# Performance work log

Hardware: AMD Instinct MI355X
Metric: run time of the kernel (lower is better)

The kernel has to match this reference:

```python
import jax, jax.numpy as jnp
import numpy as np

N_NODES = 100000
N_EDGES = 1600000
D_IN = 64
D_HID = 64
EPS = 0.0  # dgl GINConv default: init_eps=0, learn_eps=False


def setup_inputs() -> dict:
    key = jax.random.key(0)
    k1, k2, k3, k4, k5 = jax.random.split(key, 5)
    x = jax.random.normal(k1, (N_NODES, D_IN), dtype=jnp.float32)
    src = jax.random.randint(k2, (N_EDGES,), 0, N_NODES, dtype=jnp.int32)
    dst = jax.random.randint(k3, (N_EDGES,), 0, N_NODES, dtype=jnp.int32)
    # nn.Linear-style init scale
    W1 = jax.random.normal(k4, (D_IN, D_HID), dtype=jnp.float32) / np.sqrt(D_IN)
    b1 = jnp.zeros((D_HID,), dtype=jnp.float32)
    W2 = jax.random.normal(k5, (D_HID, D_HID), dtype=jnp.float32) / np.sqrt(D_HID)
    b2 = jnp.zeros((D_HID,), dtype=jnp.float32)
    return {"x": x, "src": src, "dst": dst, "W1": W1, "b1": b1, "W2": W2, "b2": b2}


def _gin_layer(h, src, dst, W, b):
    # sum-aggregate messages from src -> dst (graph SpMM), then (1+eps)*h + agg,
    # then dense linear + ReLU — matches dgl GINConv(aggregator_type='sum', activation=ReLU)
    agg = jax.ops.segment_sum(h[src], dst, num_segments=N_NODES)  # [N, D]
    return jax.nn.relu(((1.0 + EPS) * h + agg) @ W + b)


def reference(x, src, dst, W1, b1, W2, b2):
    h = _gin_layer(x, src, dst, W1, b1)
    h = _gin_layer(h, src, dst, W2, b2)
    return h
```

## Files before the change

kernel.cpp:

```cpp
#include <hip/hip_runtime.h>
#include <hip/hip_bf16.h>


#define D 64
#define ROWS_PER_BLOCK 32
#define CHSZ 8192
#define NPBS 512
#define SBSHIFT 9
#define MAXNBS 256
#define MAXNCH 512

typedef unsigned short ushort_t;

__device__ inline unsigned short f2bf(float f) {
    unsigned u = __float_as_uint(f);
    return (unsigned short)((u + 0x7fff + ((u >> 16) & 1)) >> 16);
}

__device__ inline void acc8(float* acc, uint4 v) {
    acc[0] += __uint_as_float(v.x << 16);
    acc[1] += __uint_as_float(v.x & 0xffff0000u);
    acc[2] += __uint_as_float(v.y << 16);
    acc[3] += __uint_as_float(v.y & 0xffff0000u);
    acc[4] += __uint_as_float(v.z << 16);
    acc[5] += __uint_as_float(v.z & 0xffff0000u);
    acc[6] += __uint_as_float(v.w << 16);
    acc[7] += __uint_as_float(v.w & 0xffff0000u);
}


__global__ __launch_bounds__(256) void k1_hist(const int* __restrict__ dst,
                                               int* __restrict__ hist,
                                               int n_edges, int nch, int nbs) {
    __shared__ int lh[MAXNBS];
    for (int i = threadIdx.x; i < nbs; i += 256) lh[i] = 0;
    __syncthreads();
    int base = blockIdx.x * CHSZ;
    int lim = min(CHSZ, n_edges - base);
    for (int k = threadIdx.x; k < lim; k += 256)
        atomicAdd(&lh[dst[base + k] >> SBSHIFT], 1);
    __syncthreads();
    for (int i = threadIdx.x; i < nbs; i += 256)
        hist[i * nch + blockIdx.x] = lh[i];
}

__global__ __launch_bounds__(256) void k2a_rowsum(const int* __restrict__ hist,
                                                  int* __restrict__ total,
                                                  int nch, int nbs) {
    int w = threadIdx.x >> 6;
    int lane = threadIdx.x & 63;
    int b = blockIdx.x * 4 + w;
    if (b >= nbs) return;
    const int* row = hist + (size_t)b * nch;
    int s = 0;
    for (int c = lane; c < nch; c += 64) s += row[c];
#pragma unroll
    for (int off = 32; off > 0; off >>= 1) s += __shfl_down(s, off);
    if (lane == 0) total[b] = s;
}

__global__ __launch_bounds__(256) void k2b_scan(const int* __restrict__ total,
                                                int* __restrict__ sstart,
                                                int nbs, int n_edges) {
    __shared__ int t[256];
    int tid = threadIdx.x;
    t[tid] = (tid < nbs) ? total[tid] : 0;
    __syncthreads();
    for (int off = 1; off < 256; off <<= 1) {
        int v = (tid >= off) ? t[tid - off] : 0;
        __syncthreads();
        t[tid] += v;
        __syncthreads();
    }
    if (tid < nbs) sstart[tid] = (tid == 0) ? 0 : t[tid - 1];
    if (tid == 0) sstart[nbs] = n_edges;
}

__global__ __launch_bounds__(256) void k2c_rowscan(int* __restrict__ hist,
                                                   const int* __restrict__ sstart,
                                                   int nch, int nbs) {
    __shared__ int t[MAXNCH];
    int b = blockIdx.x;
    int tid = threadIdx.x;
    int* row = hist + (size_t)b * nch;
    int nround = (nch + 255) & ~255;
    for (int i = tid; i < nround; i += 256) t[i] = (i < nch) ? row[i] : 0;
    __syncthreads();
    for (int off = 1; off < nround; off <<= 1) {
        int v[MAXNCH / 256];
        for (int i = tid, j = 0; i < nround; i += 256, ++j)
            v[j] = (i >= off) ? t[i - off] : 0;
        __syncthreads();
        for (int i = tid, j = 0; i < nround; i += 256, ++j) t[i] += v[j];
        __syncthreads();
    }
    int base = sstart[b];
    for (int i = tid; i < nch; i += 256)
        row[i] = base + ((i == 0) ? 0 : t[i - 1]);
}

__global__ __launch_bounds__(256) void k3_scatter(const int* __restrict__ src,
                                                  const int* __restrict__ dst,
                                                  const int* __restrict__ hist,
                                                  unsigned* __restrict__ tmp,
                                                  int n_edges, int nch, int nbs) {
    __shared__ int lcur[MAXNBS];
    int c = blockIdx.x;
    for (int i = threadIdx.x; i < nbs; i += 256) lcur[i] = hist[i * nch + c];
    __syncthreads();
    int base = c * CHSZ;
    int lim = min(CHSZ, n_edges - base);
    for (int k = threadIdx.x; k < lim; k += 256) {
        int d = dst[base + k];
        int s = src[base + k];
        int pos = atomicAdd(&lcur[d >> SBSHIFT], 1);
        tmp[pos] = ((unsigned)(d & (NPBS - 1)) << 18) | (unsigned)s;
    }
}

__global__ __launch_bounds__(256) void k4_fine(const unsigned* __restrict__ tmp,
                                               const int* __restrict__ sstart,
                                               int* __restrict__ esrc,
                                               int* __restrict__ offs,
                                               int n_nodes) {
    __shared__ int lcnt[NPBS];
    __shared__ int lcur[NPBS];
    __shared__ int tsum[256];

    int b = blockIdx.x;
    int tid = threadIdx.x;
    int base = sstart[b];
    int cnt = sstart[b + 1] - base;

    lcnt[tid] = 0; lcnt[tid + 256] = 0;
    __syncthreads();

    for (int i = tid; i < cnt; i += 256)
        atomicAdd(&lcnt[tmp[base + i] >> 18], 1);
    __syncthreads();

    int a0 = lcnt[2 * tid], a1 = lcnt[2 * tid + 1];
    tsum[tid] = a0 + a1;
    __syncthreads();
    for (int off = 1; off < 256; off <<= 1) {
        int v = (tid >= off) ? tsum[tid - off] : 0;
        __syncthreads();
        tsum[tid] += v;
        __syncthreads();
    }
    int ex = (tid == 0) ? 0 : tsum[tid - 1];
    lcur[2 * tid] = ex;
    lcur[2 * tid + 1] = ex + a0;

    int node = b * NPBS + 2 * tid;
    if (node <= n_nodes) offs[node] = base + ex;
    if (node + 1 <= n_nodes) offs[node + 1] = base + ex + a0;
    __syncthreads();

    for (int i = tid; i < cnt; i += 256) {
        unsigned p = tmp[base + i];
        int pos = atomicAdd(&lcur[p >> 18], 1);
        esrc[base + pos] = (int)(p & 0x3FFFFu);
    }
}


__global__ __launch_bounds__(256) void to_bf16(const float4* __restrict__ in,
                                               uint2* __restrict__ out, int n4) {
    int i = blockIdx.x * 256 + threadIdx.x;
    if (i >= n4) return;
    float4 v = in[i];
    out[i] = make_uint2((unsigned)f2bf(v.x) | ((unsigned)f2bf(v.y) << 16),
                        (unsigned)f2bf(v.z) | ((unsigned)f2bf(v.w) << 16));
}

__global__ __launch_bounds__(256) void gin_agg_bf(const uint4* __restrict__ hb,
                                                  const int* __restrict__ offs,
                                                  const int* __restrict__ esrc,
                                                  float4* __restrict__ agg,
                                                  int n_nodes) {
    int t = blockIdx.x * 256 + threadIdx.x;
    int n = t >> 2;
    if (n >= n_nodes) return;
    int c = t & 3;
    const uint4* self = hb + (size_t)n * 8 + c * 2;
    float acc[16];
#pragma unroll
    for (int j = 0; j < 16; ++j) acc[j] = 0.0f;
    uint4 sv0 = self[0], sv1 = self[1];
    acc8(acc, sv0); acc8(acc + 8, sv1);

    int i = offs[n];
    int end = offs[n + 1];
    for (; i + 4 <= end; i += 4) {
        const uint4* r0 = hb + (size_t)esrc[i]     * 8 + c * 2;
        const uint4* r1 = hb + (size_t)esrc[i + 1] * 8 + c * 2;
        const uint4* r2 = hb + (size_t)esrc[i + 2] * 8 + c * 2;
        const uint4* r3 = hb + (size_t)esrc[i + 3] * 8 + c * 2;
        uint4 a0 = r0[0], b0 = r0[1];
        uint4 a1 = r1[0], b1 = r1[1];
        uint4 a2 = r2[0], b2 = r2[1];
        uint4 a3 = r3[0], b3 = r3[1];
        acc8(acc, a0); acc8(acc + 8, b0);
        acc8(acc, a1); acc8(acc + 8, b1);
        acc8(acc, a2); acc8(acc + 8, b2);
        acc8(acc, a3); acc8(acc + 8, b3);
    }
    for (; i < end; ++i) {
        const uint4* r = hb + (size_t)esrc[i] * 8 + c * 2;
        uint4 a = r[0], b = r[1];
        acc8(acc, a); acc8(acc + 8, b);
    }

    float4* o = agg + (size_t)n * 16 + c * 4;
    o[0] = make_float4(acc[0], acc[1], acc[2], acc[3]);
    o[1] = make_float4(acc[4], acc[5], acc[6], acc[7]);
    o[2] = make_float4(acc[8], acc[9], acc[10], acc[11]);
    o[3] = make_float4(acc[12], acc[13], acc[14], acc[15]);
}

template <bool BF16OUT>
__global__ __launch_bounds__(256) void gin_mlp(const float* __restrict__ hs,
                                               const float* __restrict__ W,
                                               const float* __restrict__ b,
                                               void* __restrict__ out_,
                                               int n_nodes) {
    __shared__ float Wl[D * D];
    __shared__ float bl[D];
    __shared__ float rows[ROWS_PER_BLOCK][D];

    int tid = threadIdx.x;

    const float4* W4 = (const float4*)W;
    float4* Wl4 = (float4*)Wl;
#pragma unroll
    for (int i = 0; i < 4; ++i) Wl4[tid + 256 * i] = W4[tid + 256 * i];
    if (tid < D / 4) ((float4*)bl)[tid] = ((const float4*)b)[tid];

    size_t row0 = (size_t)blockIdx.x * ROWS_PER_BLOCK;
    const float4* hs4 = (const float4*)(hs + row0 * D);
    float4* rows4 = (float4*)rows;
#pragma unroll
    for (int i = 0; i < 2; ++i) rows4[tid + 256 * i] = hs4[tid + 256 * i];

    __syncthreads();

    int lane = tid & 63;
    int w = tid >> 6;

    float acc[8];
#pragma unroll
    for (int r = 0; r < 8; ++r) acc[r] = bl[lane];

#pragma unroll
    for (int k = 0; k < D; ++k) {
        float wv = Wl[k * D + lane];
#pragma unroll
        for (int r = 0; r < 8; ++r)
            acc[r] = fmaf(rows[w * 8 + r][k], wv, acc[r]);
    }

#pragma unroll
    for (int r = 0; r < 8; ++r) {
        float v = acc[r] > 0.0f ? acc[r] : 0.0f;
        size_t idx = (row0 + (size_t)w * 8 + r) * D + lane;
        if (BF16OUT) ((ushort_t*)out_)[idx] = f2bf(v);
        else         ((float*)out_)[idx] = v;
    }
}

extern "C" void kernel_launch(void* const* d_in, const int* in_sizes, int n_in,
                              void* d_out, int out_size, void* d_ws, size_t ws_size,
                              hipStream_t stream) {
    const float* x   = (const float*)d_in[0];
    const int*   src = (const int*)d_in[1];
    const int*   dst = (const int*)d_in[2];
    const float* W1  = (const float*)d_in[3];
    const float* b1  = (const float*)d_in[4];
    const float* W2  = (const float*)d_in[5];
    const float* b2  = (const float*)d_in[6];
    float* out = (float*)d_out;

    const int n_nodes = in_sizes[0] / D;
    const int n_edges = in_sizes[1];
    const int nch = (n_edges + CHSZ - 1) / CHSZ;
    const int nbs = (n_nodes + NPBS - 1) / NPBS;

    float*    A      = (float*)d_ws;
    ushort_t* hb     = (ushort_t*)(A + (size_t)n_nodes * D);
    int*      offs   = (int*)(hb + (size_t)n_nodes * D);
    int*      sstart = offs + (n_nodes + 1);
    int*      total  = sstart + (nbs + 1);
    int*      hist   = total + nbs;
    unsigned* tmp    = (unsigned*)(hist + (size_t)nbs * nch);
    int*      esrc   = (int*)(tmp + n_edges);

    const int agg_blocks = (n_nodes * 4 + 255) / 256;
    const int mlp_blocks = (n_nodes + ROWS_PER_BLOCK - 1) / ROWS_PER_BLOCK;
    const int cvt_blocks = (n_nodes * (D / 4) + 255) / 256;

    k1_hist<<<nch, 256, 0, stream>>>(dst, hist, n_edges, nch, nbs);
    k2a_rowsum<<<(nbs + 3) / 4, 256, 0, stream>>>(hist, total, nch, nbs);
    k2b_scan<<<1, 256, 0, stream>>>(total, sstart, nbs, n_edges);
    k2c_rowscan<<<nbs, 256, 0, stream>>>(hist, sstart, nch, nbs);
    k3_scatter<<<nch, 256, 0, stream>>>(src, dst, hist, tmp, n_edges, nch, nbs);
    k4_fine<<<nbs, 256, 0, stream>>>(tmp, sstart, esrc, offs, n_nodes);

    to_bf16<<<cvt_blocks, 256, 0, stream>>>((const float4*)x, (uint2*)hb,
                                            n_nodes * (D / 4));
    gin_agg_bf<<<agg_blocks, 256, 0, stream>>>((const uint4*)hb, offs, esrc,
                                               (float4*)A, n_nodes);
    gin_mlp<true><<<mlp_blocks, 256, 0, stream>>>(A, W1, b1, hb, n_nodes);

    gin_agg_bf<<<agg_blocks, 256, 0, stream>>>((const uint4*)hb, offs, esrc,
                                               (float4*)A, n_nodes);
    gin_mlp<false><<<mlp_blocks, 256, 0, stream>>>(A, W2, b2, out, n_nodes);
}
```

Before: 196.4 us.

## Fuse aggregation into MLP and group nodes by degree for balanced work

```diff
diff --git a/kernel.cpp b/kernel.cpp
--- a/kernel.cpp
+++ b/kernel.cpp
@@ -3,12 +3,13 @@
 
 
 #define D 64
-#define ROWS_PER_BLOCK 32
+#define RPB 32
 #define CHSZ 8192
 #define NPBS 512
 #define SBSHIFT 9
 #define MAXNBS 256
 #define MAXNCH 512
+#define DBINS 256
 
 typedef unsigned short ushort_t;
 
@@ -29,8 +30,15 @@
 }
 
 
+__global__ void zero_small(int* __restrict__ total, int* __restrict__ degcnt, int nbs) {
+    int i = threadIdx.x;
+    for (int j = i; j < nbs; j += 256) total[j] = 0;
+    for (int j = i; j < DBINS; j += 256) degcnt[j] = 0;
+}
+
 __global__ __launch_bounds__(256) void k1_hist(const int* __restrict__ dst,
                                                int* __restrict__ hist,
+                                               int* __restrict__ total,
                                                int n_edges, int nch, int nbs) {
     __shared__ int lh[MAXNBS];
     for (int i = threadIdx.x; i < nbs; i += 256) lh[i] = 0;
@@ -40,23 +48,11 @@
     for (int k = threadIdx.x; k < lim; k += 256)
         atomicAdd(&lh[dst[base + k] >> SBSHIFT], 1);
     __syncthreads();
-    for (int i = threadIdx.x; i < nbs; i += 256)
-        hist[i * nch + blockIdx.x] = lh[i];
-}
-
-__global__ __launch_bounds__(256) void k2a_rowsum(const int* __restrict__ hist,
-                                                  int* __restrict__ total,
-                                                  int nch, int nbs) {
-    int w = threadIdx.x >> 6;
-    int lane = threadIdx.x & 63;
-    int b = blockIdx.x * 4 + w;
-    if (b >= nbs) return;
-    const int* row = hist + (size_t)b * nch;
-    int s = 0;
-    for (int c = lane; c < nch; c += 64) s += row[c];
-#pragma unroll
-    for (int off = 32; off > 0; off >>= 1) s += __shfl_down(s, off);
-    if (lane == 0) total[b] = s;
+    for (int i = threadIdx.x; i < nbs; i += 256) {
+        int v = lh[i];
+        hist[i * nch + blockIdx.x] = v;
+        if (v) atomicAdd(&total[i], v);
+    }
 }
 
 __global__ __launch_bounds__(256) void k2b_scan(const int* __restrict__ total,
@@ -122,10 +118,12 @@
                                                const int* __restrict__ sstart,
                                                int* __restrict__ esrc,
                                                int* __restrict__ offs,
+                                               int* __restrict__ degcnt,
                                                int n_nodes) {
     __shared__ int lcnt[NPBS];
     __shared__ int lcur[NPBS];
     __shared__ int tsum[256];
+    __shared__ int dcnt[DBINS];
 
     int b = blockIdx.x;
     int tid = threadIdx.x;
@@ -133,6 +131,7 @@
     int cnt = sstart[b + 1] - base;
 
     lcnt[tid] = 0; lcnt[tid + 256] = 0;
+    dcnt[tid] = 0;
     __syncthreads();
 
     for (int i = tid; i < cnt; i += 256)
@@ -140,6 +139,9 @@
     __syncthreads();
 
     int a0 = lcnt[2 * tid], a1 = lcnt[2 * tid + 1];
+    int node = b * NPBS + 2 * tid;
+    if (node < n_nodes)     atomicAdd(&dcnt[min(a0, DBINS - 1)], 1);
+    if (node + 1 < n_nodes) atomicAdd(&dcnt[min(a1, DBINS - 1)], 1);
     tsum[tid] = a0 + a1;
     __syncthreads();
     for (int off = 1; off < 256; off <<= 1) {
@@ -152,16 +154,53 @@
     lcur[2 * tid] = ex;
     lcur[2 * tid + 1] = ex + a0;
 
-    int node = b * NPBS + 2 * tid;
     if (node <= n_nodes) offs[node] = base + ex;
     if (node + 1 <= n_nodes) offs[node + 1] = base + ex + a0;
     __syncthreads();
+
+    if (dcnt[tid]) atomicAdd(&degcnt[tid], dcnt[tid]);
 
     for (int i = tid; i < cnt; i += 256) {
         unsigned p = tmp[base + i];
         int pos = atomicAdd(&lcur[p >> 18], 1);
         esrc[base + pos] = (int)(p & 0x3FFFFu);
     }
+}
+
+__global__ __launch_bounds__(256) void degscan(const int* __restrict__ degcnt,
+                                               int* __restrict__ degcur) {
+    __shared__ int t[DBINS];
+    int tid = threadIdx.x;
+    t[tid] = degcnt[tid];
+    __syncthreads();
+    for (int off = 1; off < 256; off <<= 1) {
+        int v = (tid >= off) ? t[tid - off] : 0;
+        __syncthreads();
+        t[tid] += v;
+        __syncthreads();
+    }
+    degcur[tid] = (tid == 0) ? 0 : t[tid - 1];
+}
+
+__global__ __launch_bounds__(256) void degscatter(const int* __restrict__ offs,
+                                                  int* __restrict__ degcur,
+                                                  int* __restrict__ perm,
+                                                  int n_nodes) {
+    __shared__ int lcnt[DBINS];
+    __shared__ int lbase[DBINS];
+    int tid = threadIdx.x;
+    int n = blockIdx.x * 256 + tid;
+    lcnt[tid] = 0;
+    __syncthreads();
+    int bin = -1, lpos = 0;
+    if (n < n_nodes) {
+        bin = min(offs[n + 1] - offs[n], DBINS - 1);
+        lpos = atomicAdd(&lcnt[bin], 1);
+    }
+    __syncthreads();
+    if (lcnt[tid]) lbase[tid] = atomicAdd(&degcur[tid], lcnt[tid]);
+    __syncthreads();
+    if (n < n_nodes) perm[lbase[bin] + lpos] = n;
 }
 
 
@@ -174,60 +213,19 @@
                         (unsigned)f2bf(v.z) | ((unsigned)f2bf(v.w) << 16));
 }
 
-__global__ __launch_bounds__(256) void gin_agg_bf(const uint4* __restrict__ hb,
-                                                  const int* __restrict__ offs,
-                                                  const int* __restrict__ esrc,
-                                                  float4* __restrict__ agg,
-                                                  int n_nodes) {
-    int t = blockIdx.x * 256 + threadIdx.x;
-    int n = t >> 2;
-    if (n >= n_nodes) return;
-    int c = t & 3;
-    const uint4* self = hb + (size_t)n * 8 + c * 2;
-    float acc[16];
-#pragma unroll
-    for (int j = 0; j < 16; ++j) acc[j] = 0.0f;
-    uint4 sv0 = self[0], sv1 = self[1];
-    acc8(acc, sv0); acc8(acc + 8, sv1);
-
-    int i = offs[n];
-    int end = offs[n + 1];
-    for (; i + 4 <= end; i += 4) {
-        const uint4* r0 = hb + (size_t)esrc[i]     * 8 + c * 2;
-        const uint4* r1 = hb + (size_t)esrc[i + 1] * 8 + c * 2;
-        const uint4* r2 = hb + (size_t)esrc[i + 2] * 8 + c * 2;
-        const uint4* r3 = hb + (size_t)esrc[i + 3] * 8 + c * 2;
-        uint4 a0 = r0[0], b0 = r0[1];
-        uint4 a1 = r1[0], b1 = r1[1];
-        uint4 a2 = r2[0], b2 = r2[1];
-        uint4 a3 = r3[0], b3 = r3[1];
-        acc8(acc, a0); acc8(acc + 8, b0);
-        acc8(acc, a1); acc8(acc + 8, b1);
-        acc8(acc, a2); acc8(acc + 8, b2);
-        acc8(acc, a3); acc8(acc + 8, b3);
-    }
-    for (; i < end; ++i) {
-        const uint4* r = hb + (size_t)esrc[i] * 8 + c * 2;
-        uint4 a = r[0], b = r[1];
-        acc8(acc, a); acc8(acc + 8, b);
-    }
-
-    float4* o = agg + (size_t)n * 16 + c * 4;
-    o[0] = make_float4(acc[0], acc[1], acc[2], acc[3]);
-    o[1] = make_float4(acc[4], acc[5], acc[6], acc[7]);
-    o[2] = make_float4(acc[8], acc[9], acc[10], acc[11]);
-    o[3] = make_float4(acc[12], acc[13], acc[14], acc[15]);
-}
-
 template <bool BF16OUT>
-__global__ __launch_bounds__(256) void gin_mlp(const float* __restrict__ hs,
-                                               const float* __restrict__ W,
-                                               const float* __restrict__ b,
-                                               void* __restrict__ out_,
-                                               int n_nodes) {
+__global__ __launch_bounds__(256) void gin_layer(const uint4* __restrict__ hb,
+                                                 const int* __restrict__ offs,
+                                                 const int* __restrict__ esrc,
+                                                 const int* __restrict__ perm,
+                                                 const float* __restrict__ W,
+                                                 const float* __restrict__ bias,
+                                                 void* __restrict__ out_,
+                                                 int n_nodes) {
     __shared__ float Wl[D * D];
     __shared__ float bl[D];
-    __shared__ float rows[ROWS_PER_BLOCK][D];
+    __shared__ float rows[RPB][D];
+    __shared__ int pn[RPB];
 
     int tid = threadIdx.x;
 
@@ -235,35 +233,58 @@
     float4* Wl4 = (float4*)Wl;
 #pragma unroll
     for (int i = 0; i < 4; ++i) Wl4[tid + 256 * i] = W4[tid + 256 * i];
-    if (tid < D / 4) ((float4*)bl)[tid] = ((const float4*)b)[tid];
-
-    size_t row0 = (size_t)blockIdx.x * ROWS_PER_BLOCK;
-    const float4* hs4 = (const float4*)(hs + row0 * D);
-    float4* rows4 = (float4*)rows;
-#pragma unroll
-    for (int i = 0; i < 2; ++i) rows4[tid + 256 * i] = hs4[tid + 256 * i];
-
+    if (tid < D / 4) ((float4*)bl)[tid] = ((const float4*)bias)[tid];
+    if (tid < RPB) {
+        int r = blockIdx.x * RPB + tid;
+        pn[tid] = (r < n_nodes) ? perm[r] : -1;
+    }
+    __syncthreads();
+
+    int g = tid >> 3;
+    int l = tid & 7;
+    int n = pn[g];
+    float acc[8];
+#pragma unroll
+    for (int j = 0; j < 8; ++j) acc[j] = 0.0f;
+    if (n >= 0) {
+        acc8(acc, hb[(size_t)n * 8 + l]);
+        int i = offs[n];
+        int end = offs[n + 1];
+        for (; i + 4 <= end; i += 4) {
+            uint4 v0 = hb[(size_t)esrc[i]     * 8 + l];
+            uint4 v1 = hb[(size_t)esrc[i + 1] * 8 + l];
+            uint4 v2 = hb[(size_t)esrc[i + 2] * 8 + l];
+            uint4 v3 = hb[(size_t)esrc[i + 3] * 8 + l];
+            acc8(acc, v0); acc8(acc, v1); acc8(acc, v2); acc8(acc, v3);
+        }
+        for (; i < end; ++i)
+            acc8(acc, hb[(size_t)esrc[i] * 8 + l]);
+    }
+#pragma unroll
+    for (int j = 0; j < 8; ++j) rows[g][l * 8 + j] = acc[j];
     __syncthreads();
 
     int lane = tid & 63;
     int w = tid >> 6;
 
-    float acc[8];
-#pragma unroll
-    for (int r = 0; r < 8; ++r) acc[r] = bl[lane];
+    float macc[8];
+#pragma unroll
+    for (int r = 0; r < 8; ++r) macc[r] = bl[lane];
 
 #pragma unroll
     for (int k = 0; k < D; ++k) {
         float wv = Wl[k * D + lane];
 #pragma unroll
         for (int r = 0; r < 8; ++r)
-            acc[r] = fmaf(rows[w * 8 + r][k], wv, acc[r]);
+            macc[r] = fmaf(rows[w * 8 + r][k], wv, macc[r]);
     }
 
 #pragma unroll
     for (int r = 0; r < 8; ++r) {
-        float v = acc[r] > 0.0f ? acc[r] : 0.0f;
-        size_t idx = (row0 + (size_t)w * 8 + r) * D + lane;
+        int nr = pn[w * 8 + r];
+        if (nr < 0) continue;
+        float v = macc[r] > 0.0f ? macc[r] : 0.0f;
+        size_t idx = (size_t)nr * D + lane;
         if (BF16OUT) ((ushort_t*)out_)[idx] = f2bf(v);
         else         ((float*)out_)[idx] = v;
     }
@@ -286,33 +307,36 @@
     const int nch = (n_edges + CHSZ - 1) / CHSZ;
     const int nbs = (n_nodes + NPBS - 1) / NPBS;
 
-    float*    A      = (float*)d_ws;
-    ushort_t* hb     = (ushort_t*)(A + (size_t)n_nodes * D);
-    int*      offs   = (int*)(hb + (size_t)n_nodes * D);
+    ushort_t* xb     = (ushort_t*)d_ws;
+    ushort_t* h1b    = xb + (size_t)n_nodes * D;
+    int*      offs   = (int*)(h1b + (size_t)n_nodes * D);
     int*      sstart = offs + (n_nodes + 1);
     int*      total  = sstart + (nbs + 1);
-    int*      hist   = total + nbs;
-    unsigned* tmp    = (unsigned*)(hist + (size_t)nbs * nch);
+    int*      degcnt = total + nbs;
+    int*      degcur = degcnt + DBINS;
+    int*      hist   = degcur + DBINS;
+    int*      perm   = hist + (size_t)nbs * nch;
+    unsigned* tmp    = (unsigned*)(perm + n_nodes);
     int*      esrc   = (int*)(tmp + n_edges);
 
-    const int agg_blocks = (n_nodes * 4 + 255) / 256;
-    const int mlp_blocks = (n_nodes + ROWS_PER_BLOCK - 1) / ROWS_PER_BLOCK;
+    const int layer_blocks = (n_nodes + RPB - 1) / RPB;
     const int cvt_blocks = (n_nodes * (D / 4) + 255) / 256;
-
-    k1_hist<<<nch, 256, 0, stream>>>(dst, hist, n_edges, nch, nbs);
-    k2a_rowsum<<<(nbs + 3) / 4, 256, 0, stream>>>(hist, total, nch, nbs);
+    const int nscat_blocks = (n_nodes + 255) / 256;
+
+    zero_small<<<1, 256, 0, stream>>>(total, degcnt, nbs);
+    k1_hist<<<nch, 256, 0, stream>>>(dst, hist, total, n_edges, nch, nbs);
     k2b_scan<<<1, 256, 0, stream>>>(total, sstart, nbs, n_edges);
     k2c_rowscan<<<nbs, 256, 0, stream>>>(hist, sstart, nch, nbs);
     k3_scatter<<<nch, 256, 0, stream>>>(src, dst, hist, tmp, n_edges, nch, nbs);
-    k4_fine<<<nbs, 256, 0, stream>>>(tmp, sstart, esrc, offs, n_nodes);
-
-    to_bf16<<<cvt_blocks, 256, 0, stream>>>((const float4*)x, (uint2*)hb,
+    k4_fine<<<nbs, 256, 0, stream>>>(tmp, sstart, esrc, offs, degcnt, n_nodes);
+    degscan<<<1, 256, 0, stream>>>(degcnt, degcur);
+    degscatter<<<nscat_blocks, 256, 0, stream>>>(offs, degcur, perm, n_nodes);
+
+    to_bf16<<<cvt_blocks, 256, 0, stream>>>((const float4*)x, (uint2*)xb,
                                             n_nodes * (D / 4));
-    gin_agg_bf<<<agg_blocks, 256, 0, stream>>>((const uint4*)hb, offs, esrc,
-                                               (float4*)A, n_nodes);
-    gin_mlp<true><<<mlp_blocks, 256, 0, stream>>>(A, W1, b1, hb, n_nodes);
-
-    gin_agg_bf<<<agg_blocks, 256, 0, stream>>>((const uint4*)hb, offs, esrc,
-                                               (float4*)A, n_nodes);
-    gin_mlp<false><<<mlp_blocks, 256, 0, stream>>>(A, W2, b2, out, n_nodes);
-}
+    gin_layer<true><<<layer_blocks, 256, 0, stream>>>((const uint4*)xb, offs, esrc,
+                                                      perm, W1, b1, h1b, n_nodes);
+
+    gin_layer<false><<<layer_blocks, 256, 0, stream>>>((const uint4*)h1b, offs, esrc,
+                                                       perm, W2, b2, out, n_nodes);
+}
```

Result: slower. 462.0 us (+135.2%).

## Sort nodes by in-degree for load-balanced aggregation; fold row-sum into histogram

Applied to the files above, without the earlier changes.

```diff
diff --git a/kernel.cpp b/kernel.cpp
--- a/kernel.cpp
+++ b/kernel.cpp
@@ -9,6 +9,7 @@
 #define SBSHIFT 9
 #define MAXNBS 256
 #define MAXNCH 512
+#define DBINS 256
 
 typedef unsigned short ushort_t;
 
@@ -29,8 +30,15 @@
 }
 
 
+__global__ void zero_small(int* __restrict__ total, int* __restrict__ degcnt, int nbs) {
+    int i = threadIdx.x;
+    for (int j = i; j < nbs; j += 256) total[j] = 0;
+    for (int j = i; j < DBINS; j += 256) degcnt[j] = 0;
+}
+
 __global__ __launch_bounds__(256) void k1_hist(const int* __restrict__ dst,
                                                int* __restrict__ hist,
+                                               int* __restrict__ total,
                                                int n_edges, int nch, int nbs) {
     __shared__ int lh[MAXNBS];
     for (int i = threadIdx.x; i < nbs; i += 256) lh[i] = 0;
@@ -40,23 +48,11 @@
     for (int k = threadIdx.x; k < lim; k += 256)
         atomicAdd(&lh[dst[base + k] >> SBSHIFT], 1);
     __syncthreads();
-    for (int i = threadIdx.x; i < nbs; i += 256)
-        hist[i * nch + blockIdx.x] = lh[i];
-}
-
-__global__ __launch_bounds__(256) void k2a_rowsum(const int* __restrict__ hist,
-                                                  int* __restrict__ total,
-                                                  int nch, int nbs) {
-    int w = threadIdx.x >> 6;
-    int lane = threadIdx.x & 63;
-    int b = blockIdx.x * 4 + w;
-    if (b >= nbs) return;
-    const int* row = hist + (size_t)b * nch;
-    int s = 0;
-    for (int c = lane; c < nch; c += 64) s += row[c];
-#pragma unroll
-    for (int off = 32; off > 0; off >>= 1) s += __shfl_down(s, off);
-    if (lane == 0) total[b] = s;
+    for (int i = threadIdx.x; i < nbs; i += 256) {
+        int v = lh[i];
+        hist[i * nch + blockIdx.x] = v;
+        if (v) atomicAdd(&total[i], v);
+    }
 }
 
 __global__ __launch_bounds__(256) void k2b_scan(const int* __restrict__ total,
@@ -122,10 +118,12 @@
                                                const int* __restrict__ sstart,
                                                int* __restrict__ esrc,
                                                int* __restrict__ offs,
+                                               int* __restrict__ degcnt,
                                                int n_nodes) {
     __shared__ int lcnt[NPBS];
     __shared__ int lcur[NPBS];
     __shared__ int tsum[256];
+    __shared__ int dcnt[DBINS];
 
     int b = blockIdx.x;
     int tid = threadIdx.x;
@@ -133,6 +131,7 @@
     int cnt = sstart[b + 1] - base;
 
     lcnt[tid] = 0; lcnt[tid + 256] = 0;
+    dcnt[tid] = 0;
     __syncthreads();
 
     for (int i = tid; i < cnt; i += 256)
@@ -140,6 +139,9 @@
     __syncthreads();
 
     int a0 = lcnt[2 * tid], a1 = lcnt[2 * tid + 1];
+    int node = b * NPBS + 2 * tid;
+    if (node < n_nodes)     atomicAdd(&dcnt[min(a0, DBINS - 1)], 1);
+    if (node + 1 < n_nodes) atomicAdd(&dcnt[min(a1, DBINS - 1)], 1);
     tsum[tid] = a0 + a1;
     __syncthreads();
     for (int off = 1; off < 256; off <<= 1) {
@@ -152,16 +154,53 @@
     lcur[2 * tid] = ex;
     lcur[2 * tid + 1] = ex + a0;
 
-    int node = b * NPBS + 2 * tid;
     if (node <= n_nodes) offs[node] = base + ex;
     if (node + 1 <= n_nodes) offs[node + 1] = base + ex + a0;
     __syncthreads();
+
+    if (dcnt[tid]) atomicAdd(&degcnt[tid], dcnt[tid]);
 
     for (int i = tid; i < cnt; i += 256) {
         unsigned p = tmp[base + i];
         int pos = atomicAdd(&lcur[p >> 18], 1);
         esrc[base + pos] = (int)(p & 0x3FFFFu);
     }
+}
+
+__global__ __launch_bounds__(256) void degscan(const int* __restrict__ degcnt,
+                                               int* __restrict__ degcur) {
+    __shared__ int t[DBINS];
+    int tid = threadIdx.x;
+    t[tid] = degcnt[tid];
+    __syncthreads();
+    for (int off = 1; off < 256; off <<= 1) {
+        int v = (tid >= off) ? t[tid - off] : 0;
+        __syncthreads();
+        t[tid] += v;
+        __syncthreads();
+    }
+    degcur[tid] = (tid == 0) ? 0 : t[tid - 1];
+}
+
+__global__ __launch_bounds__(256) void degscatter(const int* __restrict__ offs,
+                                                  int* __restrict__ degcur,
+                                                  int* __restrict__ perm,
+                                                  int n_nodes) {
+    __shared__ int lcnt[DBINS];
+    __shared__ int lbase[DBINS];
+    int tid = threadIdx.x;
+    int n = blockIdx.x * 256 + tid;
+    lcnt[tid] = 0;
+    __syncthreads();
+    int bin = -1, lpos = 0;
+    if (n < n_nodes) {
+        bin = min(offs[n + 1] - offs[n], DBINS - 1);
+        lpos = atomicAdd(&lcnt[bin], 1);
+    }
+    __syncthreads();
+    if (lcnt[tid]) lbase[tid] = atomicAdd(&degcur[tid], lcnt[tid]);
+    __syncthreads();
+    if (n < n_nodes) perm[lbase[bin] + lpos] = n;
 }
 
 
@@ -177,11 +216,13 @@
 __global__ __launch_bounds__(256) void gin_agg_bf(const uint4* __restrict__ hb,
                                                   const int* __restrict__ offs,
                                                   const int* __restrict__ esrc,
+                                                  const int* __restrict__ perm,
                                                   float4* __restrict__ agg,
                                                   int n_nodes) {
     int t = blockIdx.x * 256 + threadIdx.x;
-    int n = t >> 2;
-    if (n >= n_nodes) return;
+    int nidx = t >> 2;
+    if (nidx >= n_nodes) return;
+    int n = perm[nidx];
     int c = t & 3;
     const uint4* self = hb + (size_t)n * 8 + c * 2;
     float acc[16];
@@ -291,28 +332,34 @@
     int*      offs   = (int*)(hb + (size_t)n_nodes * D);
     int*      sstart = offs + (n_nodes + 1);
     int*      total  = sstart + (nbs + 1);
-    int*      hist   = total + nbs;
-    unsigned* tmp    = (unsigned*)(hist + (size_t)nbs * nch);
+    int*      degcnt = total + nbs;
+    int*      degcur = degcnt + DBINS;
+    int*      hist   = degcur + DBINS;
+    int*      perm   = hist + (size_t)nbs * nch;
+    unsigned* tmp    = (unsigned*)(perm + n_nodes);
     int*      esrc   = (int*)(tmp + n_edges);
 
     const int agg_blocks = (n_nodes * 4 + 255) / 256;
     const int mlp_blocks = (n_nodes + ROWS_PER_BLOCK - 1) / ROWS_PER_BLOCK;
     const int cvt_blocks = (n_nodes * (D / 4) + 255) / 256;
-
-    k1_hist<<<nch, 256, 0, stream>>>(dst, hist, n_edges, nch, nbs);
-    k2a_rowsum<<<(nbs + 3) / 4, 256, 0, stream>>>(hist, total, nch, nbs);
+    const int nscat_blocks = (n_nodes + 255) / 256;
+
+    zero_small<<<1, 256, 0, stream>>>(total, degcnt, nbs);
+    k1_hist<<<nch, 256, 0, stream>>>(dst, hist, total, n_edges, nch, nbs);
     k2b_scan<<<1, 256, 0, stream>>>(total, sstart, nbs, n_edges);
     k2c_rowscan<<<nbs, 256, 0, stream>>>(hist, sstart, nch, nbs);
     k3_scatter<<<nch, 256, 0, stream>>>(src, dst, hist, tmp, n_edges, nch, nbs);
-    k4_fine<<<nbs, 256, 0, stream>>>(tmp, sstart, esrc, offs, n_nodes);
+    k4_fine<<<nbs, 256, 0, stream>>>(tmp, sstart, esrc, offs, degcnt, n_nodes);
+    degscan<<<1, 256, 0, stream>>>(degcnt, degcur);
+    degscatter<<<nscat_blocks, 256, 0, stream>>>(offs, degcur, perm, n_nodes);
 
     to_bf16<<<cvt_blocks, 256, 0, stream>>>((const float4*)x, (uint2*)hb,
                                             n_nodes * (D / 4));
     gin_agg_bf<<<agg_blocks, 256, 0, stream>>>((const uint4*)hb, offs, esrc,
-                                               (float4*)A, n_nodes);
+                                               perm, (float4*)A, n_nodes);
     gin_mlp<true><<<mlp_blocks, 256, 0, stream>>>(A, W1, b1, hb, n_nodes);
 
     gin_agg_bf<<<agg_blocks, 256, 0, stream>>>((const uint4*)hb, offs, esrc,
-                                               (float4*)A, n_nodes);
+                                               perm, (float4*)A, n_nodes);
     gin_mlp<false><<<mlp_blocks, 256, 0, stream>>>(A, W2, b2, out, n_nodes);
 }
```

Result: slower. 217.5 us (+10.7%).

## Store aggregates as bf16 and fold the histogram prefix into fewer launches

Applied to the files above, without the earlier changes.

```diff
diff --git a/kernel.cpp b/kernel.cpp
--- a/kernel.cpp
+++ b/kernel.cpp
@@ -28,9 +28,29 @@
     acc[7] += __uint_as_float(v.w & 0xffff0000u);
 }
 
+__device__ inline void unpack8(float* v, uint4 u) {
+    v[0] = __uint_as_float(u.x << 16); v[1] = __uint_as_float(u.x & 0xffff0000u);
+    v[2] = __uint_as_float(u.y << 16); v[3] = __uint_as_float(u.y & 0xffff0000u);
+    v[4] = __uint_as_float(u.z << 16); v[5] = __uint_as_float(u.z & 0xffff0000u);
+    v[6] = __uint_as_float(u.w << 16); v[7] = __uint_as_float(u.w & 0xffff0000u);
+}
+
+
+__global__ __launch_bounds__(256) void to_bf16z(const float4* __restrict__ in,
+                                                uint2* __restrict__ out, int n4,
+                                                int* __restrict__ total, int nbs) {
+    int i = blockIdx.x * 256 + threadIdx.x;
+    if (blockIdx.x == 0)
+        for (int j = threadIdx.x; j < nbs; j += 256) total[j] = 0;
+    if (i >= n4) return;
+    float4 v = in[i];
+    out[i] = make_uint2((unsigned)f2bf(v.x) | ((unsigned)f2bf(v.y) << 16),
+                        (unsigned)f2bf(v.z) | ((unsigned)f2bf(v.w) << 16));
+}
 
 __global__ __launch_bounds__(256) void k1_hist(const int* __restrict__ dst,
                                                int* __restrict__ hist,
+                                               int* __restrict__ total,
                                                int n_edges, int nch, int nbs) {
     __shared__ int lh[MAXNBS];
     for (int i = threadIdx.x; i < nbs; i += 256) lh[i] = 0;
@@ -40,48 +60,36 @@
     for (int k = threadIdx.x; k < lim; k += 256)
         atomicAdd(&lh[dst[base + k] >> SBSHIFT], 1);
     __syncthreads();
-    for (int i = threadIdx.x; i < nbs; i += 256)
-        hist[i * nch + blockIdx.x] = lh[i];
-}
-
-__global__ __launch_bounds__(256) void k2a_rowsum(const int* __restrict__ hist,
-                                                  int* __restrict__ total,
-                                                  int nch, int nbs) {
-    int w = threadIdx.x >> 6;
-    int lane = threadIdx.x & 63;
-    int b = blockIdx.x * 4 + w;
-    if (b >= nbs) return;
-    const int* row = hist + (size_t)b * nch;
-    int s = 0;
-    for (int c = lane; c < nch; c += 64) s += row[c];
-#pragma unroll
-    for (int off = 32; off > 0; off >>= 1) s += __shfl_down(s, off);
-    if (lane == 0) total[b] = s;
-}
-
-__global__ __launch_bounds__(256) void k2b_scan(const int* __restrict__ total,
-                                                int* __restrict__ sstart,
-                                                int nbs, int n_edges) {
-    __shared__ int t[256];
-    int tid = threadIdx.x;
-    t[tid] = (tid < nbs) ? total[tid] : 0;
-    __syncthreads();
-    for (int off = 1; off < 256; off <<= 1) {
-        int v = (tid >= off) ? t[tid - off] : 0;
-        __syncthreads();
-        t[tid] += v;
-        __syncthreads();
-    }
-    if (tid < nbs) sstart[tid] = (tid == 0) ? 0 : t[tid - 1];
-    if (tid == 0) sstart[nbs] = n_edges;
+    for (int i = threadIdx.x; i < nbs; i += 256) {
+        int v = lh[i];
+        hist[i * nch + blockIdx.x] = v;
+        if (v) atomicAdd(&total[i], v);
+    }
 }
 
 __global__ __launch_bounds__(256) void k2c_rowscan(int* __restrict__ hist,
-                                                   const int* __restrict__ sstart,
-                                                   int nch, int nbs) {
+                                                   const int* __restrict__ total,
+                                                   int* __restrict__ sstart,
+                                                   int nch, int nbs, int n_edges) {
+    __shared__ int tt[256];
     __shared__ int t[MAXNCH];
     int b = blockIdx.x;
     int tid = threadIdx.x;
+
+    tt[tid] = (tid < nbs) ? total[tid] : 0;
+    __syncthreads();
+    for (int off = 1; off < 256; off <<= 1) {
+        int v = (tid >= off) ? tt[tid - off] : 0;
+        __syncthreads();
+        tt[tid] += v;
+        __syncthreads();
+    }
+    int base = (b == 0) ? 0 : tt[b - 1];
+    if (tid == 0) {
+        sstart[b] = base;
+        if (b == 0) sstart[nbs] = n_edges;
+    }
+
     int* row = hist + (size_t)b * nch;
     int nround = (nch + 255) & ~255;
     for (int i = tid; i < nround; i += 256) t[i] = (i < nch) ? row[i] : 0;
@@ -94,7 +102,6 @@
         for (int i = tid, j = 0; i < nround; i += 256, ++j) t[i] += v[j];
         __syncthreads();
     }
-    int base = sstart[b];
     for (int i = tid; i < nch; i += 256)
         row[i] = base + ((i == 0) ? 0 : t[i - 1]);
 }
@@ -165,19 +172,10 @@
 }
 
 
-__global__ __launch_bounds__(256) void to_bf16(const float4* __restrict__ in,
-                                               uint2* __restrict__ out, int n4) {
-    int i = blockIdx.x * 256 + threadIdx.x;
-    if (i >= n4) return;
-    float4 v = in[i];
-    out[i] = make_uint2((unsigned)f2bf(v.x) | ((unsigned)f2bf(v.y) << 16),
-                        (unsigned)f2bf(v.z) | ((unsigned)f2bf(v.w) << 16));
-}
-
 __global__ __launch_bounds__(256) void gin_agg_bf(const uint4* __restrict__ hb,
                                                   const int* __restrict__ offs,
                                                   const int* __restrict__ esrc,
-                                                  float4* __restrict__ agg,
+                                                  uint4* __restrict__ aggb,
                                                   int n_nodes) {
     int t = blockIdx.x * 256 + threadIdx.x;
     int n = t >> 2;
@@ -212,22 +210,29 @@
         acc8(acc, a); acc8(acc + 8, b);
     }
 
-    float4* o = agg + (size_t)n * 16 + c * 4;
-    o[0] = make_float4(acc[0], acc[1], acc[2], acc[3]);
-    o[1] = make_float4(acc[4], acc[5], acc[6], acc[7]);
-    o[2] = make_float4(acc[8], acc[9], acc[10], acc[11]);
-    o[3] = make_float4(acc[12], acc[13], acc[14], acc[15]);
-}
-
+    uint4 o0, o1;
+    o0.x = (unsigned)f2bf(acc[0])  | ((unsigned)f2bf(acc[1])  << 16);
+    o0.y = (unsigned)f2bf(acc[2])  | ((unsigned)f2bf(acc[3])  << 16);
+    o0.z = (unsigned)f2bf(acc[4])  | ((unsigned)f2bf(acc[5])  << 16);
+    o0.w = (unsigned)f2bf(acc[6])  | ((unsigned)f2bf(acc[7])  << 16);
+    o1.x = (unsigned)f2bf(acc[8])  | ((unsigned)f2bf(acc[9])  << 16);
+    o1.y = (unsigned)f2bf(acc[10]) | ((unsigned)f2bf(acc[11]) << 16);
+    o1.z = (unsigned)f2bf(acc[12]) | ((unsigned)f2bf(acc[13]) << 16);
+    o1.w = (unsigned)f2bf(acc[14]) | ((unsigned)f2bf(acc[15]) << 16);
+    aggb[(size_t)n * 8 + c * 2]     = o0;
+    aggb[(size_t)n * 8 + c * 2 + 1] = o1;
+}
+
+#define RSTRIDE (D + 4)
 template <bool BF16OUT>
-__global__ __launch_bounds__(256) void gin_mlp(const float* __restrict__ hs,
+__global__ __launch_bounds__(256) void gin_mlp(const uint4* __restrict__ hs,
                                                const float* __restrict__ W,
                                                const float* __restrict__ b,
                                                void* __restrict__ out_,
                                                int n_nodes) {
     __shared__ float Wl[D * D];
     __shared__ float bl[D];
-    __shared__ float rows[ROWS_PER_BLOCK][D];
+    __shared__ float rows[ROWS_PER_BLOCK * RSTRIDE];
 
     int tid = threadIdx.x;
 
@@ -238,11 +243,16 @@
     if (tid < D / 4) ((float4*)bl)[tid] = ((const float4*)b)[tid];
 
     size_t row0 = (size_t)blockIdx.x * ROWS_PER_BLOCK;
-    const float4* hs4 = (const float4*)(hs + row0 * D);
-    float4* rows4 = (float4*)rows;
-#pragma unroll
-    for (int i = 0; i < 2; ++i) rows4[tid + 256 * i] = hs4[tid + 256 * i];
-
+    {
+        uint4 u = hs[row0 * 8 + tid];
+        float v[8];
+        unpack8(v, u);
+        int r = tid >> 3;
+        int col = (tid & 7) * 8;
+        float* dstp = rows + r * RSTRIDE + col;
+#pragma unroll
+        for (int j = 0; j < 8; ++j) dstp[j] = v[j];
+    }
     __syncthreads();
 
     int lane = tid & 63;
@@ -257,7 +267,7 @@
         float wv = Wl[k * D + lane];
 #pragma unroll
         for (int r = 0; r < 8; ++r)
-            acc[r] = fmaf(rows[w * 8 + r][k], wv, acc[r]);
+            acc[r] = fmaf(rows[(w * 8 + r) * RSTRIDE + k], wv, acc[r]);
     }
 
 #pragma unroll
@@ -286,8 +296,8 @@
     const int nch = (n_edges + CHSZ - 1) / CHSZ;
     const int nbs = (n_nodes + NPBS - 1) / NPBS;
 
-    float*    A      = (float*)d_ws;
-    ushort_t* hb     = (ushort_t*)(A + (size_t)n_nodes * D);
+    ushort_t* Ab     = (ushort_t*)d_ws;
+    ushort_t* hb     = Ab + (size_t)n_nodes * D;
     int*      offs   = (int*)(hb + (size_t)n_nodes * D);
     int*      sstart = offs + (n_nodes + 1);
     int*      total  = sstart + (nbs + 1);
@@ -299,20 +309,20 @@
     const int mlp_blocks = (n_nodes + ROWS_PER_BLOCK - 1) / ROWS_PER_BLOCK;
     const int cvt_blocks = (n_nodes * (D / 4) + 255) / 256;
 
-    k1_hist<<<nch, 256, 0, stream>>>(dst, hist, n_edges, nch, nbs);
-    k2a_rowsum<<<(nbs + 3) / 4, 256, 0, stream>>>(hist, total, nch, nbs);
-    k2b_scan<<<1, 256, 0, stream>>>(total, sstart, nbs, n_edges);
-    k2c_rowscan<<<nbs, 256, 0, stream>>>(hist, sstart, nch, nbs);
+    to_bf16z<<<cvt_blocks, 256, 0, stream>>>((const float4*)x, (uint2*)hb,
+                                             n_nodes * (D / 4), total, nbs);
+    k1_hist<<<nch, 256, 0, stream>>>(dst, hist, total, n_edges, nch, nbs);
+    k2c_rowscan<<<nbs, 256, 0, stream>>>(hist, total, sstart, nch, nbs, n_edges);
     k3_scatter<<<nch, 256, 0, stream>>>(src, dst, hist, tmp, n_edges, nch, nbs);
     k4_fine<<<nbs, 256, 0, stream>>>(tmp, sstart, esrc, offs, n_nodes);
 
-    to_bf16<<<cvt_blocks, 256, 0, stream>>>((const float4*)x, (uint2*)hb,
-                                            n_nodes * (D / 4));
     gin_agg_bf<<<agg_blocks, 256, 0, stream>>>((const uint4*)hb, offs, esrc,
-                                               (float4*)A, n_nodes);
-    gin_mlp<true><<<mlp_blocks, 256, 0, stream>>>(A, W1, b1, hb, n_nodes);
+                                               (uint4*)Ab, n_nodes);
+    gin_mlp<true><<<mlp_blocks, 256, 0, stream>>>((const uint4*)Ab, W1, b1,
+                                                  hb, n_nodes);
 
     gin_agg_bf<<<agg_blocks, 256, 0, stream>>>((const uint4*)hb, offs, esrc,
-                                               (float4*)A, n_nodes);
-    gin_mlp<false><<<mlp_blocks, 256, 0, stream>>>(A, W2, b2, out, n_nodes);
-}
+                                               (uint4*)Ab, n_nodes);
+    gin_mlp<false><<<mlp_blocks, 256, 0, stream>>>((const uint4*)Ab, W2, b2,
+                                                   out, n_nodes);
+}
```

Result: no change. 195.2 us (-0.6%).
